# Kernel optimization log

Measured on AMD Instinct MI355X. Metric: run time of the kernel, lower is better.

Reference implementation:

```python
import jax, jax.numpy as jnp
import numpy as np

N_CODES = 1024
DIM = 64
COMMITMENT = 0.25


def setup_inputs() -> dict:
    key = jax.random.key(0)
    k1, k2 = jax.random.split(key)
    z = jax.random.normal(k1, (32, DIM, 64, 64), dtype=jnp.float32)  # [B, C, H, W]
    codebook = jax.random.uniform(
        k2, (N_CODES, DIM), dtype=jnp.float32,
        minval=-1.0 / N_CODES, maxval=1.0 / N_CODES,
    )
    return {"z": z, "codebook": codebook}


def reference(z, codebook):
    B, C, H, W = z.shape
    # [B, C, H, W] -> [B*H*W, C]
    z_flat = jnp.transpose(z, (0, 2, 3, 1)).reshape(-1, C)
    # Pairwise squared distances: ||z||^2 + ||e||^2 - 2 z.e  -> [N, n_codes]
    dists = (
        jnp.sum(z_flat * z_flat, axis=1, keepdims=True)
        + jnp.sum(codebook * codebook, axis=1)
        - 2.0 * (z_flat @ codebook.T)
    )
    indices = jnp.argmin(dists, axis=1)  # [N]
    z_q = codebook[indices].reshape(B, H, W, C).transpose(0, 3, 1, 2)  # [B, C, H, W]

    commit_loss = jnp.mean((jax.lax.stop_gradient(z_q) - z) ** 2)
    codebook_loss = jnp.mean((z_q - jax.lax.stop_gradient(z)) ** 2)
    vq_loss = codebook_loss + COMMITMENT * commit_loss

    # Straight-through estimator
    z_q_st = z + jax.lax.stop_gradient(z_q - z)

    # Codebook usage fraction (jit-friendly equivalent of len(unique)/n_codes)
    counts = jnp.zeros((codebook.shape[0],), dtype=jnp.int32).at[indices].add(1)
    usage = jnp.mean((counts > 0).astype(jnp.float32))

    return z_q_st, vq_loss, usage, indices.reshape(B, H, W)
```

## Files before the change

### kernel.cpp

```cpp
#include <hip/hip_runtime.h>

#define NCODES 1024
#define DIM 64
#define HW 4096
#define CHW 262144
#define NPOS 131072
#define NELEM 8388608
#define TAU 4e-5f

#define WS_LOSS 0
#define WS_CNT 4
#define WS_FLAGS 256
#define WS_BSWZ 8192
#define WS_CBN 270336
#define WS_LIST 274432

typedef __attribute__((ext_vector_type(8))) short bf16x8;
typedef __attribute__((ext_vector_type(4))) float f32x4;
typedef __attribute__((ext_vector_type(4))) unsigned int u32x4;

__device__ __forceinline__ unsigned short f2bf(float x) {
  unsigned u = __float_as_uint(x);
  return (unsigned short)((u + 0x7FFFu + ((u >> 16) & 1u)) >> 16);
}
__device__ __forceinline__ float bf2f(unsigned short h) {
  return __uint_as_float(((unsigned)h) << 16);
}
__device__ __forceinline__ unsigned fxf(float d) {
  unsigned u = __float_as_uint(d);
  return (u & 0x80000000u) ? ~u : (u | 0x80000000u);
}
__device__ __forceinline__ float fxi(unsigned u) {
  unsigned v = (u & 0x80000000u) ? (u ^ 0x80000000u) : ~u;
  return __uint_as_float(v);
}

__global__ __launch_bounds__(256) void vq_prep(const float* __restrict__ cb,
                                               unsigned short* __restrict__ bswz,
                                               float* __restrict__ cbn) {
  int t = blockIdx.x * 256 + threadIdx.x;
  int n = t >> 6, k = t & 63;
  float v = cb[n * 64 + k];
  unsigned short h = f2bf(v);
  unsigned short lo = f2bf(v - bf2f(h));
  int i = n >> 4, lmod = n & 15;
  int q = k >> 5, kr = k & 31;
  int e = ((kr >> 4) << 2) | (kr & 3);
  int l = lmod | (((kr >> 2) & 3) << 4);
  bswz[(((i * 2 + 0) * 2 + q) * 64 + l) * 8 + e] = h;
  bswz[(((i * 2 + 1) * 2 + q) * 64 + l) * 8 + e] = lo;
  if (k == 0) {
    const float* ep = cb + n * 64;
    float s = 0.f;
#pragma unroll
    for (int c = 0; c < 64; ++c) s = fmaf(ep[c], ep[c], s);
    cbn[n] = s;
  }
}

__global__ __launch_bounds__(512, 4) void vq_phaseA(
    const float* __restrict__ z, const float* __restrict__ cb,
    const unsigned short* __restrict__ bswz, const float* __restrict__ cbn,
    float* __restrict__ out_zq, float* __restrict__ out_idx,
    float* __restrict__ loss, unsigned* __restrict__ cnt,
    unsigned* __restrict__ list, int* __restrict__ flags) {
  const int tid = threadIdx.x, w = tid >> 6, l = tid & 63;
  const int l15 = l & 15, lg = (l >> 4) & 3;
  const int posbase = blockIdx.x * 256;
  const int b = posbase >> 12;
  const int hwb = posbase & 4095;

  bf16x8 A[2][2][2];
#pragma unroll
  for (int s = 0; s < 2; ++s) {
    const float* zp = z + (size_t)b * CHW + (hwb + w * 32 + s * 16 + l15);
#pragma unroll
    for (int q = 0; q < 2; ++q) {
      bf16x8 ah, al;
#pragma unroll
      for (int e = 0; e < 8; ++e) {
        int c = q * 32 + ((e >> 2) << 4) + (lg << 2) + (e & 3);
        float v = zp[c * HW];
        unsigned short h = f2bf(v);
        ah[e] = (short)h;
        al[e] = (short)f2bf(v - bf2f(h));
      }
      A[s][q][0] = ah;
      A[s][q][1] = al;
    }
  }

  unsigned long long mk[2][4];
  unsigned m2[2][4];
#pragma unroll
  for (int s = 0; s < 2; ++s)
#pragma unroll
    for (int r = 0; r < 4; ++r) { mk[s][r] = ~0ull; m2[s][r] = 0xFFFFFFFFu; }

  const u32x4* B = (const u32x4*)bswz;
  for (int i = 0; i < 64; ++i) {
    bf16x8 b00 = __builtin_bit_cast(bf16x8, B[(i * 4 + 0) * 64 + l]);
    bf16x8 b01 = __builtin_bit_cast(bf16x8, B[(i * 4 + 1) * 64 + l]);
    bf16x8 b10 = __builtin_bit_cast(bf16x8, B[(i * 4 + 2) * 64 + l]);
    bf16x8 b11 = __builtin_bit_cast(bf16x8, B[(i * 4 + 3) * 64 + l]);
    float cbnv = cbn[i * 16 + l15];
    unsigned nb = (unsigned)(i * 16 + l15);
#pragma unroll
    for (int s = 0; s < 2; ++s) {
      f32x4 C = {0.f, 0.f, 0.f, 0.f};
      C = __builtin_amdgcn_mfma_f32_16x16x32_bf16(A[s][0][0], b00, C, 0, 0, 0);
      C = __builtin_amdgcn_mfma_f32_16x16x32_bf16(A[s][1][0], b01, C, 0, 0, 0);
      C = __builtin_amdgcn_mfma_f32_16x16x32_bf16(A[s][0][0], b10, C, 0, 0, 0);
      C = __builtin_amdgcn_mfma_f32_16x16x32_bf16(A[s][1][0], b11, C, 0, 0, 0);
      C = __builtin_amdgcn_mfma_f32_16x16x32_bf16(A[s][0][1], b00, C, 0, 0, 0);
      C = __builtin_amdgcn_mfma_f32_16x16x32_bf16(A[s][1][1], b01, C, 0, 0, 0);
#pragma unroll
      for (int r = 0; r < 4; ++r) {
        float d = fmaf(C[r], -2.0f, cbnv);
        unsigned u = fxf(d);
        unsigned long long key = ((unsigned long long)u << 32) | nb;
        bool lt = key < mk[s][r];
        unsigned loser = lt ? (unsigned)(mk[s][r] >> 32) : u;
        if (lt) mk[s][r] = key;
        m2[s][r] = min(m2[s][r], loser);
      }
    }
  }

#pragma unroll
  for (int s = 0; s < 2; ++s)
#pragma unroll
    for (int r = 0; r < 4; ++r) {
      unsigned long long k = mk[s][r];
      unsigned mm2 = m2[s][r];
#pragma unroll
      for (int st = 1; st < 16; st <<= 1) {
        unsigned long long ok = __shfl_xor(k, st, 64);
        unsigned o2 = __shfl_xor(mm2, st, 64);
        unsigned loser = (unsigned)((k < ok ? ok : k) >> 32);
        k = k < ok ? k : ok;
        mm2 = min(min(mm2, o2), loser);
      }
      mk[s][r] = k;
      m2[s][r] = mm2;
    }

  __shared__ unsigned res[256];
  if (l15 == 0) {
#pragma unroll
    for (int s = 0; s < 2; ++s)
#pragma unroll
      for (int r = 0; r < 4; ++r) {
        unsigned u1 = (unsigned)(mk[s][r] >> 32);
        float gap = fxi(m2[s][r]) - fxi(u1);
        unsigned bj = (unsigned)(mk[s][r] & 0xFFFFFFFFull);
        res[w * 32 + s * 16 + lg * 4 + r] = bj | ((gap <= TAU) ? 0x80000000u : 0u);
      }
  }
  __syncthreads();

  const int pl = tid & 255, half = tid >> 8;
  unsigned pk = res[pl];
  unsigned bj = pk & 1023u;
  int pos = posbase + pl;
  float lsum = 0.f;
  if (pk & 0x80000000u) {
    if (half == 0) {
      unsigned idx = atomicAdd(cnt, 1u);
      list[idx] = (unsigned)pos;
    }
  } else {
    if (half == 0) {
      out_idx[pos] = (float)bj;
      flags[bj] = 1;
    }
    const float* zp = z + (size_t)b * CHW + (pos & 4095);
    const float* eb = cb + bj * 64;
    float* op = out_zq + (size_t)b * CHW + (pos & 4095);
#pragma unroll
    for (int cc = 0; cc < 32; ++cc) {
      int c = half * 32 + cc;
      float zv = zp[c * HW];
      float e = eb[c];
      float diff = e - zv;
      lsum = fmaf(diff, diff, lsum);
      op[c * HW] = zv + diff;
    }
  }
  for (int off = 32; off; off >>= 1) lsum += __shfl_down(lsum, off, 64);
  __shared__ float wsum[8];
  if (l == 0) wsum[w] = lsum;
  __syncthreads();
  if (tid == 0) {
    float t2 = 0.f;
#pragma unroll
    for (int i2 = 0; i2 < 8; ++i2) t2 += wsum[i2];
    atomicAdd(loss, t2);
  }
}

__global__ __launch_bounds__(256) void vq_phaseB(
    const float* __restrict__ z, const float* __restrict__ cb,
    const float* __restrict__ cbn, float* __restrict__ out_zq,
    float* __restrict__ out_idx, float* __restrict__ loss,
    const unsigned* __restrict__ cnt, const unsigned* __restrict__ list,
    int* __restrict__ flags) {
  const unsigned total = *cnt;
  const int t = threadIdx.x;
  const int l = t & 63, w = t >> 6;
  __shared__ float zsh[64];
  __shared__ unsigned long long wred[4];
  __shared__ unsigned bjsh;

  for (unsigned i = blockIdx.x; i < total; i += gridDim.x) {
    const int pos = (int)list[i];
    const int b = pos >> 12, hw = pos & 4095;
    const float* zp = z + (size_t)b * CHW + hw;
    __syncthreads();
    if (t < 64) zsh[t] = zp[t * HW];
    __syncthreads();

    float A = 0.f;
#pragma unroll
    for (int c = 0; c < 64; ++c) A = fmaf(zsh[c], zsh[c], A);

    unsigned long long best = ~0ull;
#pragma unroll
    for (int jj = 0; jj < 4; ++jj) {
      const int j = jj * 256 + t;
      const float* ej = cb + j * 64;
      float d0 = 0.f, d1 = 0.f, d2 = 0.f, d3 = 0.f;
#pragma unroll
      for (int k = 0; k < 64; k += 4) {
        d0 = fmaf(zsh[k + 0], ej[k + 0], d0);
        d1 = fmaf(zsh[k + 1], ej[k + 1], d1);
        d2 = fmaf(zsh[k + 2], ej[k + 2], d2);
        d3 = fmaf(zsh[k + 3], ej[k + 3], d3);
      }
      float dot = (d0 + d1) + (d2 + d3);
      float dist = (A + cbn[j]) - 2.0f * dot;
      unsigned long long key =
          ((unsigned long long)fxf(dist) << 32) | (unsigned)j;
      best = best < key ? best : key;
    }

    for (int st = 1; st < 64; st <<= 1) {
      unsigned long long ok = __shfl_xor(best, st, 64);
      best = best < ok ? best : ok;
    }
    if (l == 0) wred[w] = best;
    __syncthreads();
    if (t == 0) {
      unsigned long long ka = wred[0] < wred[1] ? wred[0] : wred[1];
      unsigned long long kb = wred[2] < wred[3] ? wred[2] : wred[3];
      unsigned long long km = ka < kb ? ka : kb;
      unsigned bj = (unsigned)(km & 0xFFFFFFFFull);
      bjsh = bj;
      out_idx[pos] = (float)bj;
      flags[bj] = 1;
    }
    __syncthreads();
    const unsigned bj = bjsh;

    float lsum = 0.f;
    if (t < 64) {
      float zv = zsh[t];
      float e = cb[bj * 64 + t];
      float diff = e - zv;
      lsum = fmaf(diff, diff, 0.f);
      out_zq[(size_t)b * CHW + (size_t)t * HW + hw] = zv + diff;
      for (int off = 32; off; off >>= 1) lsum += __shfl_down(lsum, off, 64);
      if (t == 0) atomicAdd(loss, lsum);
    }
  }
}

__global__ __launch_bounds__(1024) void vq_finalize(
    const int* __restrict__ flags, const float* __restrict__ loss,
    float* __restrict__ out_scalars) {
  __shared__ int cnt_[16];
  int t = threadIdx.x;
  int f = flags[t];
  for (int off = 32; off; off >>= 1) f += __shfl_down(f, off, 64);
  int lane = t & 63, wid = t >> 6;
  if (lane == 0) cnt_[wid] = f;
  __syncthreads();
  if (t == 0) {
    int c = 0;
#pragma unroll
    for (int i = 0; i < 16; ++i) c += cnt_[i];
    out_scalars[0] = 1.25f * (*loss) / (float)NELEM;
    out_scalars[1] = (float)c / (float)NCODES;
  }
}

extern "C" void kernel_launch(void* const* d_in, const int* in_sizes, int n_in,
                              void* d_out, int out_size, void* d_ws, size_t ws_size,
                              hipStream_t stream) {
  const float* z = (const float*)d_in[0];
  const float* cb = (const float*)d_in[1];
  float* out = (float*)d_out;

  char* ws = (char*)d_ws;
  float* loss = (float*)(ws + WS_LOSS);
  unsigned* cnt = (unsigned*)(ws + WS_CNT);
  int* flags = (int*)(ws + WS_FLAGS);
  unsigned short* bswz = (unsigned short*)(ws + WS_BSWZ);
  float* cbn = (float*)(ws + WS_CBN);
  unsigned* list = (unsigned*)(ws + WS_LIST);

  hipMemsetAsync(d_ws, 0, 8192, stream);
  vq_prep<<<256, 256, 0, stream>>>(cb, bswz, cbn);
  vq_phaseA<<<512, 512, 0, stream>>>(z, cb, bswz, cbn, out, out + NELEM + 2,
                                     loss, cnt, list, flags);
  vq_phaseB<<<2048, 256, 0, stream>>>(z, cb, cbn, out, out + NELEM + 2, loss,
                                      cnt, list, flags);
  vq_finalize<<<1, NCODES, 0, stream>>>(flags, loss, out + NELEM);
}
```

Measured before the change: 257.6 us.

## Batch fallback positions per lane in phaseB and use float argmin in phaseA

Phase A's running argmin now tracks float best, second-best and index separately instead of packed 64-bit keys, which makes the per-MFMA comparison cheaper. Phase B is restructured so each lane handles one ambiguous position and each of 8 waves scans a 128-code slice of the codebook. Partial results are merged through shared memory, and the z_q write-back is split across waves by channel. This replaces one block per position with a block-wide reduction per position, aiming to amortise the reduction and sync overhead. In exchange it uses heavy register pressure (64 z values per lane) and leaves many lanes idle when the fallback list is short.

After: 219.1 us. 1.18x faster.

```diff
diff --git a/kernel.cpp b/kernel.cpp
--- a/kernel.cpp
+++ b/kernel.cpp
@@ -29,10 +29,6 @@
 __device__ __forceinline__ unsigned fxf(float d) {
   unsigned u = __float_as_uint(d);
   return (u & 0x80000000u) ? ~u : (u | 0x80000000u);
-}
-__device__ __forceinline__ float fxi(unsigned u) {
-  unsigned v = (u & 0x80000000u) ? (u ^ 0x80000000u) : ~u;
-  return __uint_as_float(v);
 }
 
 __global__ __launch_bounds__(256) void vq_prep(const float* __restrict__ cb,
@@ -90,12 +86,14 @@
     }
   }
 
-  unsigned long long mk[2][4];
-  unsigned m2[2][4];
+  float bd[2][4], b2[2][4];
+  unsigned bi[2][4];
 #pragma unroll
   for (int s = 0; s < 2; ++s)
 #pragma unroll
-    for (int r = 0; r < 4; ++r) { mk[s][r] = ~0ull; m2[s][r] = 0xFFFFFFFFu; }
+    for (int r = 0; r < 4; ++r) {
+      bd[s][r] = 3.4e38f; b2[s][r] = 3.4e38f; bi[s][r] = 0;
+    }
 
   const u32x4* B = (const u32x4*)bswz;
   for (int i = 0; i < 64; ++i) {
@@ -117,46 +115,39 @@
 #pragma unroll
       for (int r = 0; r < 4; ++r) {
         float d = fmaf(C[r], -2.0f, cbnv);
-        unsigned u = fxf(d);
-        unsigned long long key = ((unsigned long long)u << 32) | nb;
-        bool lt = key < mk[s][r];
-        unsigned loser = lt ? (unsigned)(mk[s][r] >> 32) : u;
-        if (lt) mk[s][r] = key;
-        m2[s][r] = min(m2[s][r], loser);
-      }
-    }
-  }
-
+        bool lt = d < bd[s][r];
+        float loser = lt ? bd[s][r] : d;
+        b2[s][r] = fminf(b2[s][r], loser);
+        bd[s][r] = fminf(bd[s][r], d);
+        bi[s][r] = lt ? nb : bi[s][r];
+      }
+    }
+  }
+
+  __shared__ unsigned res[256];
 #pragma unroll
   for (int s = 0; s < 2; ++s)
 #pragma unroll
     for (int r = 0; r < 4; ++r) {
-      unsigned long long k = mk[s][r];
-      unsigned mm2 = m2[s][r];
+      float d = bd[s][r], s2 = b2[s][r];
+      unsigned idx = bi[s][r];
 #pragma unroll
       for (int st = 1; st < 16; st <<= 1) {
-        unsigned long long ok = __shfl_xor(k, st, 64);
-        unsigned o2 = __shfl_xor(mm2, st, 64);
-        unsigned loser = (unsigned)((k < ok ? ok : k) >> 32);
-        k = k < ok ? k : ok;
-        mm2 = min(min(mm2, o2), loser);
-      }
-      mk[s][r] = k;
-      m2[s][r] = mm2;
-    }
-
-  __shared__ unsigned res[256];
-  if (l15 == 0) {
-#pragma unroll
-    for (int s = 0; s < 2; ++s)
-#pragma unroll
-      for (int r = 0; r < 4; ++r) {
-        unsigned u1 = (unsigned)(mk[s][r] >> 32);
-        float gap = fxi(m2[s][r]) - fxi(u1);
-        unsigned bj = (unsigned)(mk[s][r] & 0xFFFFFFFFull);
-        res[w * 32 + s * 16 + lg * 4 + r] = bj | ((gap <= TAU) ? 0x80000000u : 0u);
-      }
-  }
+        float od = __shfl_xor(d, st, 64);
+        unsigned oi = __shfl_xor(idx, st, 64);
+        float o2 = __shfl_xor(s2, st, 64);
+        bool take = (od < d) || (od == d && oi < idx);
+        float loser = take ? d : od;
+        s2 = fminf(fminf(s2, o2), loser);
+        d = take ? od : d;
+        idx = take ? oi : idx;
+      }
+      if (l15 == 0) {
+        float gap = s2 - d;
+        res[w * 32 + s * 16 + lg * 4 + r] =
+            idx | ((gap <= TAU) ? 0x80000000u : 0u);
+      }
+    }
   __syncthreads();
 
   const int pl = tid & 255, half = tid >> 8;
@@ -199,78 +190,100 @@
   }
 }
 
-__global__ __launch_bounds__(256) void vq_phaseB(
+template <int W>
+__device__ __forceinline__ void epilogue8(const float* __restrict__ eb,
+                                          const float zr[DIM],
+                                          float* __restrict__ op,
+                                          float& lsum) {
+#pragma unroll
+  for (int cc = 0; cc < 8; ++cc) {
+    const int c = W * 8 + cc;
+    float e = eb[c];
+    float diff = e - zr[c];
+    lsum = fmaf(diff, diff, lsum);
+    op[c * HW] = zr[c] + diff;
+  }
+}
+
+__global__ __launch_bounds__(512, 2) void vq_phaseB(
     const float* __restrict__ z, const float* __restrict__ cb,
     const float* __restrict__ cbn, float* __restrict__ out_zq,
     float* __restrict__ out_idx, float* __restrict__ loss,
     const unsigned* __restrict__ cnt, const unsigned* __restrict__ list,
     int* __restrict__ flags) {
   const unsigned total = *cnt;
-  const int t = threadIdx.x;
-  const int l = t & 63, w = t >> 6;
-  __shared__ float zsh[64];
-  __shared__ unsigned long long wred[4];
-  __shared__ unsigned bjsh;
-
-  for (unsigned i = blockIdx.x; i < total; i += gridDim.x) {
-    const int pos = (int)list[i];
+  const int t = threadIdx.x, w = t >> 6, l = t & 63;
+  __shared__ unsigned long long keys[8][64];
+  __shared__ float wsum[8];
+
+  for (unsigned base = blockIdx.x * 64u; base < total; base += 2048u * 64u) {
+    const bool active = (base + (unsigned)l) < total;
+    const int pos = active ? (int)list[base + l] : 0;
     const int b = pos >> 12, hw = pos & 4095;
     const float* zp = z + (size_t)b * CHW + hw;
-    __syncthreads();
-    if (t < 64) zsh[t] = zp[t * HW];
-    __syncthreads();
-
+
+    float zr[DIM];
+#pragma unroll
+    for (int c = 0; c < DIM; ++c) zr[c] = zp[c * HW];
     float A = 0.f;
 #pragma unroll
-    for (int c = 0; c < 64; ++c) A = fmaf(zsh[c], zsh[c], A);
-
-    unsigned long long best = ~0ull;
-#pragma unroll
-    for (int jj = 0; jj < 4; ++jj) {
-      const int j = jj * 256 + t;
+    for (int c = 0; c < DIM; ++c) A = fmaf(zr[c], zr[c], A);
+
+    const int j0 = __builtin_amdgcn_readfirstlane(w * 128);
+    float best = 3.4e38f;
+    int bestj = j0;
+    for (int jj = 0; jj < 128; ++jj) {
+      const int j = j0 + jj;
       const float* ej = cb + j * 64;
       float d0 = 0.f, d1 = 0.f, d2 = 0.f, d3 = 0.f;
 #pragma unroll
       for (int k = 0; k < 64; k += 4) {
-        d0 = fmaf(zsh[k + 0], ej[k + 0], d0);
-        d1 = fmaf(zsh[k + 1], ej[k + 1], d1);
-        d2 = fmaf(zsh[k + 2], ej[k + 2], d2);
-        d3 = fmaf(zsh[k + 3], ej[k + 3], d3);
+        d0 = fmaf(zr[k + 0], ej[k + 0], d0);
+        d1 = fmaf(zr[k + 1], ej[k + 1], d1);
+        d2 = fmaf(zr[k + 2], ej[k + 2], d2);
+        d3 = fmaf(zr[k + 3], ej[k + 3], d3);
       }
       float dot = (d0 + d1) + (d2 + d3);
       float dist = (A + cbn[j]) - 2.0f * dot;
-      unsigned long long key =
-          ((unsigned long long)fxf(dist) << 32) | (unsigned)j;
-      best = best < key ? best : key;
-    }
-
-    for (int st = 1; st < 64; st <<= 1) {
-      unsigned long long ok = __shfl_xor(best, st, 64);
-      best = best < ok ? best : ok;
-    }
-    if (l == 0) wred[w] = best;
+      if (dist < best) { best = dist; bestj = j; }
+    }
+
+    __syncthreads();
+    keys[w][l] = ((unsigned long long)fxf(best) << 32) | (unsigned)bestj;
+    __syncthreads();
+    unsigned long long km = keys[0][l];
+#pragma unroll
+    for (int ww = 1; ww < 8; ++ww) {
+      unsigned long long k2 = keys[ww][l];
+      km = km < k2 ? km : k2;
+    }
+    const unsigned bj = (unsigned)(km & 0xFFFFFFFFull);
+
+    float lsum = 0.f;
+    if (active) {
+      const float* eb = cb + bj * 64;
+      float* op = out_zq + (size_t)b * CHW + hw;
+      if (w == 0)      epilogue8<0>(eb, zr, op, lsum);
+      else if (w == 1) epilogue8<1>(eb, zr, op, lsum);
+      else if (w == 2) epilogue8<2>(eb, zr, op, lsum);
+      else if (w == 3) epilogue8<3>(eb, zr, op, lsum);
+      else if (w == 4) epilogue8<4>(eb, zr, op, lsum);
+      else if (w == 5) epilogue8<5>(eb, zr, op, lsum);
+      else if (w == 6) epilogue8<6>(eb, zr, op, lsum);
+      else             epilogue8<7>(eb, zr, op, lsum);
+      if (w == 0) {
+        out_idx[pos] = (float)bj;
+        flags[bj] = 1;
+      }
+    }
+    for (int off = 32; off; off >>= 1) lsum += __shfl_down(lsum, off, 64);
+    if (l == 0) wsum[w] = lsum;
     __syncthreads();
     if (t == 0) {
-      unsigned long long ka = wred[0] < wred[1] ? wred[0] : wred[1];
-      unsigned long long kb = wred[2] < wred[3] ? wred[2] : wred[3];
-      unsigned long long km = ka < kb ? ka : kb;
-      unsigned bj = (unsigned)(km & 0xFFFFFFFFull);
-      bjsh = bj;
-      out_idx[pos] = (float)bj;
-      flags[bj] = 1;
-    }
-    __syncthreads();
-    const unsigned bj = bjsh;
-
-    float lsum = 0.f;
-    if (t < 64) {
-      float zv = zsh[t];
-      float e = cb[bj * 64 + t];
-      float diff = e - zv;
-      lsum = fmaf(diff, diff, 0.f);
-      out_zq[(size_t)b * CHW + (size_t)t * HW + hw] = zv + diff;
-      for (int off = 32; off; off >>= 1) lsum += __shfl_down(lsum, off, 64);
-      if (t == 0) atomicAdd(loss, lsum);
+      float t2 = 0.f;
+#pragma unroll
+      for (int i2 = 0; i2 < 8; ++i2) t2 += wsum[i2];
+      atomicAdd(loss, t2);
     }
   }
 }
@@ -313,7 +326,7 @@
   vq_prep<<<256, 256, 0, stream>>>(cb, bswz, cbn);
   vq_phaseA<<<512, 512, 0, stream>>>(z, cb, bswz, cbn, out, out + NELEM + 2,
                                      loss, cnt, list, flags);
-  vq_phaseB<<<2048, 256, 0, stream>>>(z, cb, cbn, out, out + NELEM + 2, loss,
+  vq_phaseB<<<2048, 512, 0, stream>>>(z, cb, cbn, out, out + NELEM + 2, loss,
                                       cnt, list, flags);
   vq_finalize<<<1, NCODES, 0, stream>>>(flags, loss, out + NELEM);
 }
```
